# Kernel optimization log

Measured on AMD Instinct MI355X. Metric: run time of the kernel, lower is better.

## Reference

```python
import jax, jax.numpy as jnp
import numpy as np

B, T, C = 1, 2048, 2048
H, KH, HD = 16, 4, 128  # n_head, n_kv_head, head_dim
ROPE_BASE = 10000.0


def setup_inputs() -> dict:
    key = jax.random.key(0)
    ks = jax.random.split(key, 5)
    s = 0.02
    return {
        "x": jax.random.normal(ks[0], (B, T, C), jnp.float32),
        "Wq": jax.random.normal(ks[1], (C, H * HD), jnp.float32) * s,
        "Wk": jax.random.normal(ks[2], (C, KH * HD), jnp.float32) * s,
        "Wv": jax.random.normal(ks[3], (C, KH * HD), jnp.float32) * s,
        "Wo": jax.random.normal(ks[4], (H * HD, C), jnp.float32) * s,
        "position_ids": jnp.arange(T, dtype=jnp.int32),
    }


def _rotate_half(a):
    h = a.shape[-1] // 2
    return jnp.concatenate([-a[..., h:], a[..., :h]], axis=-1)


def reference(x, Wq, Wk, Wv, Wo, position_ids):
    b, t, c = x.shape
    n_rep = H // KH
    # projections -> [B, heads, T, HD]
    q = (x @ Wq).reshape(b, t, H, HD).transpose(0, 2, 1, 3)
    k = (x @ Wk).reshape(b, t, KH, HD).transpose(0, 2, 1, 3)
    v = (x @ Wv).reshape(b, t, KH, HD).transpose(0, 2, 1, 3)
    # rotary embedding cache [T, HD]
    inv_freq = 1.0 / (ROPE_BASE ** (jnp.arange(0, HD, 2, dtype=jnp.float32) / HD))
    pos = jnp.arange(t, dtype=jnp.float32)
    freqs = pos[:, None] * inv_freq[None, :]
    emb = jnp.concatenate([freqs, freqs], axis=-1)
    cos = jnp.cos(emb)[position_ids][None, None]  # [1,1,T,HD]
    sin = jnp.sin(emb)[position_ids][None, None]
    q = q * cos + _rotate_half(q) * sin
    k = k * cos + _rotate_half(k) * sin
    # GQA: group query heads instead of materializing repeated K/V
    qg = q.reshape(b, KH, n_rep, t, HD)
    scale = jnp.float32(1.0 / np.sqrt(HD))
    scores = jnp.einsum('bgrtd,bgsd->bgrts', qg, k) * scale
    causal = jnp.tril(jnp.ones((t, t), dtype=bool))
    scores = jnp.where(causal, scores, jnp.float32(-1e30))
    p = jax.nn.softmax(scores, axis=-1)
    y = jnp.einsum('bgrts,bgsd->bgrtd', p, v)
    y = y.reshape(b, H, t, HD).transpose(0, 2, 1, 3).reshape(b, t, H * HD)
    return y @ Wo
```

## Files before the change

kernel.cpp:

```cpp
#include <hip/hip_runtime.h>

typedef unsigned short u16;
using bf16x8 = __attribute__((ext_vector_type(8))) short;
using f32x4  = __attribute__((ext_vector_type(4))) float;

#define GLD16(g, l)                                                            \
  __builtin_amdgcn_global_load_lds(                                            \
      (const __attribute__((address_space(1))) void*)(g),                      \
      (__attribute__((address_space(3))) void*)(l), 16, 0, 0)

__device__ __forceinline__ u16 f2b(float x) {
  union { float f; unsigned u; } v; v.f = x;
  unsigned r = v.u + 0x7FFF + ((v.u >> 16) & 1);
  return (u16)(r >> 16);
}
__device__ __forceinline__ float b2f(u16 x) {
  union { unsigned u; float f; } v; v.u = (unsigned)x << 16; return v.f;
}

__global__ void cast_bf16_kernel(const float* __restrict__ in,
                                 u16* __restrict__ out, int n4) {
  int i = blockIdx.x * blockDim.x + threadIdx.x;
  int stride = gridDim.x * blockDim.x;
  for (; i < n4; i += stride) {
    float4 v = ((const float4*)in)[i];
    ushort4 o;
    o.x = f2b(v.x); o.y = f2b(v.y); o.z = f2b(v.z); o.w = f2b(v.w);
    ((ushort4*)out)[i] = o;
  }
}

__global__ void transpose_all_w_kernel(const float* __restrict__ Wq,
                                       const float* __restrict__ Wk,
                                       const float* __restrict__ Wv,
                                       const float* __restrict__ Wo,
                                       u16* __restrict__ Wqkv_bt,
                                       u16* __restrict__ Wo_bt) {
  __shared__ float tile[32][33];
  const int bx = blockIdx.x, k0 = blockIdx.y * 32;
  const int tx = threadIdx.x, ty = threadIdx.y;
  const float* src; int srcN, n0s; u16* dst; int dstRow0;
  if (bx < 64)      { src = Wq; srcN = 2048; n0s = bx * 32;        dst = Wqkv_bt; dstRow0 = bx * 32; }
  else if (bx < 80) { src = Wk; srcN = 512;  n0s = (bx - 64) * 32; dst = Wqkv_bt; dstRow0 = 2048 + (bx - 64) * 32; }
  else if (bx < 96) { src = Wv; srcN = 512;  n0s = (bx - 80) * 32; dst = Wqkv_bt; dstRow0 = 2560 + (bx - 80) * 32; }
  else              { src = Wo; srcN = 2048; n0s = (bx - 96) * 32; dst = Wo_bt;   dstRow0 = (bx - 96) * 32; }
#pragma unroll
  for (int r = 0; r < 4; r++)
    tile[ty + r * 8][tx] = src[(size_t)(k0 + ty + r * 8) * srcN + n0s + tx];
  __syncthreads();
#pragma unroll
  for (int r = 0; r < 4; r++)
    dst[(size_t)(dstRow0 + ty + r * 8) * 2048 + k0 + tx] = f2b(tile[tx][ty + r * 8]);
}

__global__ void transpose_v_kernel(const u16* __restrict__ src,
                                   u16* __restrict__ dst) {
  __shared__ u16 tile[32][33];
  int h = blockIdx.z;
  int t0 = blockIdx.x * 32, d0 = blockIdx.y * 32;
  const u16* s = src + (size_t)h * 2048 * 128;
  u16* d = dst + (size_t)h * 128 * 2048;
  int tx = threadIdx.x, ty = threadIdx.y;
#pragma unroll
  for (int r = 0; r < 4; r++)
    tile[ty + r * 8][tx] = s[(size_t)(t0 + ty + r * 8) * 128 + d0 + tx];
  __syncthreads();
#pragma unroll
  for (int r = 0; r < 4; r++)
    d[(size_t)(d0 + ty + r * 8) * 2048 + t0 + tx] = tile[tx][ty + r * 8];
}

__global__ __launch_bounds__(256, 2)
void gemm_bt_128(const u16* __restrict__ A, const u16* __restrict__ Bt,
                 float* __restrict__ C, int M, int N, int K) {
  __shared__ u16 As[4][128 * 32];
  __shared__ u16 Bs[4][128 * 32];
  const int tid = threadIdx.x;
  const int lane = tid & 63;
  const int w = tid >> 6;
  const int wr = w >> 1, wc = w & 1;
  const int m0 = blockIdx.y * 128, n0 = blockIdx.x * 128;

  f32x4 acc[4][4] = {};

  const int srow = tid >> 2, skg = tid & 3;
  const u16* Ag0 = A + (size_t)(m0 + srow) * K + skg * 8;
  const u16* Ag1 = A + (size_t)(m0 + 64 + srow) * K + skg * 8;
  const u16* Bg0 = Bt + (size_t)(n0 + srow) * K + skg * 8;
  const u16* Bg1 = Bt + (size_t)(n0 + 64 + srow) * K + skg * 8;

  const int l0 = tid * 8, l1 = (256 + tid) * 8;
  u16 *pa0 = As[0], *pa1 = As[1], *pa2 = As[2], *pa3 = As[3];
  u16 *pb0 = Bs[0], *pb1 = Bs[1], *pb2 = Bs[2], *pb3 = Bs[3];

#define GSTAGE(k0v, pa, pb)                                                    \
  {                                                                            \
    GLD16(Ag0 + (k0v), (pa) + l0);                                             \
    GLD16(Ag1 + (k0v), (pa) + l1);                                             \
    GLD16(Bg0 + (k0v), (pb) + l0);                                             \
    GLD16(Bg1 + (k0v), (pb) + l1);                                             \
  }

  GSTAGE(0, pa0, pb0);
  GSTAGE(32, pa1, pb1);

  const int frow = lane & 15, fk = (lane >> 4) * 8;
  const int nk = K >> 5;

  for (int i = 0; i < nk; ++i) {
    if (i + 2 < nk) {
      GSTAGE((i + 2) * 32, pa2, pb2);
      asm volatile("s_waitcnt vmcnt(8)" ::: "memory");
    } else if (i + 1 < nk) {
      asm volatile("s_waitcnt vmcnt(4)" ::: "memory");
    } else {
      asm volatile("s_waitcnt vmcnt(0)" ::: "memory");
    }
    __builtin_amdgcn_s_barrier();
    __builtin_amdgcn_sched_barrier(0);
    bf16x8 av[4], bv[4];
#pragma unroll
    for (int m = 0; m < 4; m++)
      av[m] = *(const bf16x8*)(pa0 + (wr * 64 + m * 16 + frow) * 32 + fk);
#pragma unroll
    for (int n = 0; n < 4; n++)
      bv[n] = *(const bf16x8*)(pb0 + (wc * 64 + n * 16 + frow) * 32 + fk);
#pragma unroll
    for (int m = 0; m < 4; m++)
#pragma unroll
      for (int n = 0; n < 4; n++)
        acc[m][n] =
            __builtin_amdgcn_mfma_f32_16x16x32_bf16(av[m], bv[n], acc[m][n], 0, 0, 0);
    u16* t;
    t = pa0; pa0 = pa1; pa1 = pa2; pa2 = pa3; pa3 = t;
    t = pb0; pb0 = pb1; pb1 = pb2; pb2 = pb3; pb3 = t;
  }
#undef GSTAGE

  const int crow = (lane >> 4) * 4, ccol = lane & 15;
#pragma unroll
  for (int m = 0; m < 4; m++)
#pragma unroll
    for (int n = 0; n < 4; n++)
#pragma unroll
      for (int r = 0; r < 4; r++)
        C[(size_t)(m0 + wr * 64 + m * 16 + crow + r) * N +
          (n0 + wc * 64 + n * 16 + ccol)] = acc[m][n][r];
}

__global__ void rope_kernel(const float* __restrict__ QKV,
                            const int* __restrict__ pos, u16* __restrict__ Qb,
                            u16* __restrict__ Kb, u16* __restrict__ Vb) {
  __shared__ float sc_[64], cc_[64];
  const int t = blockIdx.x, tid = threadIdx.x;
  const float p = (float)pos[t];
  const float* row = QKV + (size_t)t * 3072;
  const float qscale = 0.08838834764831845f;
  const float c0 = -0.015625f * 13.287712379549449f;
  if (tid < 64) {
    float ang = p * exp2f((float)tid * c0);
    sc_[tid] = sinf(ang);
    cc_[tid] = cosf(ang);
  }
  __syncthreads();
#pragma unroll
  for (int i = 0; i < 4; i++) {
    int idx = tid + i * 256;
    int head = idx >> 6, d = idx & 63;
    float s = sc_[d], c = cc_[d];
    float a0 = row[head * 128 + d], a1 = row[head * 128 + d + 64];
    Qb[((size_t)head * 2048 + t) * 128 + d] = f2b((a0 * c - a1 * s) * qscale);
    Qb[((size_t)head * 2048 + t) * 128 + d + 64] = f2b((a1 * c + a0 * s) * qscale);
  }
  {
    int head = tid >> 6, d = tid & 63;
    float s = sc_[d], c = cc_[d];
    float a0 = row[2048 + head * 128 + d], a1 = row[2048 + head * 128 + d + 64];
    Kb[((size_t)head * 2048 + t) * 128 + d] = f2b(a0 * c - a1 * s);
    Kb[((size_t)head * 2048 + t) * 128 + d + 64] = f2b(a1 * c + a0 * s);
  }
#pragma unroll
  for (int i = 0; i < 2; i++) {
    int e = tid + i * 256;
    int kh = e >> 7, d = e & 127;
    Vb[((size_t)kh * 2048 + t) * 128 + d] = f2b(row[2560 + e]);
  }
}

__global__ __launch_bounds__(256, 2)
void attn_kernel(const u16* __restrict__ Qb, const u16* __restrict__ Kb,
                 const u16* __restrict__ Vtb, u16* __restrict__ Op,
                 float* __restrict__ ml) {
  __shared__ u16 Ks[2][64 * 128];
  __shared__ u16 Vs[2][128 * 64];
  __shared__ u16 Ps[4][16 * 64];
  const int tid = threadIdx.x, lane = tid & 63, w = tid >> 6;
  const int h = blockIdx.y, g = h >> 2;
  const int z = blockIdx.z;
  const int frow = lane & 15, fgrp = lane >> 4;
  const int t0 = blockIdx.x;
  const int t1 = 31 - t0;
  const int c0 = (t0 >= z) ? ((t0 - z) >> 1) + 1 : 0;
  const int c1 = ((t1 - z) >> 1) + 1;
  const int nit = c0 + c1;

  const u16* Kg = Kb + (size_t)g * 2048 * 128;
  const u16* Vg = Vtb + (size_t)g * 128 * 2048;

#define STAGE(j0v, B)                                                          \
  {                                                                            \
    _Pragma("unroll")                                                          \
    for (int i = 0; i < 4; i++) {                                              \
      int p = tid + i * 256;                                                   \
      int kr = p >> 4, kc = (p & 15) ^ (kr & 7);                               \
      GLD16(Kg + (size_t)((j0v) + kr) * 128 + kc * 8, &Ks[B][p * 8]);          \
      int vr = p >> 3, vc = (p & 7) ^ (vr & 7);                                \
      GLD16(Vg + (size_t)vr * 2048 + (j0v) + vc * 8, &Vs[B][p * 8]);           \
    }                                                                          \
  }

#define FLUSH()                                                                \
  {                                                                            \
    _Pragma("unroll")                                                          \
    for (int r = 0; r < 4; r++) {                                              \
      float inv = lrow[r] > 0.f ? 1.0f / lrow[r] : 0.f;                        \
      int t = qw + fgrp * 4 + r;                                               \
      _Pragma("unroll")                                                        \
      for (int db = 0; db < 8; db++)                                           \
        Op[(size_t)z * 4194304 + (size_t)t * 2048 + h * 128 + db * 16 + frow] =\
            f2b(o[db][r] * inv);                                               \
      if (frow == 0) {                                                         \
        int mi = (((z * 16 + h) * 2048) + t) * 2;                              \
        ml[mi] = mrow[r]; ml[mi + 1] = lrow[r];                                \
      }                                                                        \
    }                                                                          \
  }

  int qw = t0 * 64 + w * 16;
  bf16x8 qf[4];
  {
    const u16* Qrow = Qb + ((size_t)h * 2048 + (qw + frow)) * 128 + fgrp * 8;
#pragma unroll
    for (int kf = 0; kf < 4; kf++) qf[kf] = *(const bf16x8*)(Qrow + kf * 32);
  }

  f32x4 o[8] = {};
  float mrow[4], lrow[4];
#pragma unroll
  for (int r = 0; r < 4; r++) { mrow[r] = -1e30f; lrow[r] = 0.f; }

  STAGE(z * 64, 0);
  __syncthreads();

  for (int it = 0; it < nit; ++it) {
    const int buf = it & 1;
    if (it + 1 < nit) {
      const int itn = it + 1;
      const int jn = (itn < c0) ? z + 2 * itn : z + 2 * (itn - c0);
      STAGE(jn * 64, buf ^ 1);
    }
    if (it == c0) {
      FLUSH();
#pragma unroll
      for (int db = 0; db < 8; db++)
#pragma unroll
        for (int r = 0; r < 4; r++) o[db][r] = 0.f;
#pragma unroll
      for (int r = 0; r < 4; r++) { mrow[r] = -1e30f; lrow[r] = 0.f; }
      qw = t1 * 64 + w * 16;
      const u16* Qrow = Qb + ((size_t)h * 2048 + (qw + frow)) * 128 + fgrp * 8;
#pragma unroll
      for (int kf = 0; kf < 4; kf++) qf[kf] = *(const bf16x8*)(Qrow + kf * 32);
    }
    const int pass = (it < c0) ? 0 : 1;
    const int j = (pass == 0) ? z + 2 * it : z + 2 * (it - c0);
    const bool diag = (pass == 0) ? (j == t0) : (j == t1);

    f32x4 sc[4] = {};
#pragma unroll
    for (int c = 0; c < 4; c++)
#pragma unroll
      for (int kf = 0; kf < 4; kf++) {
        int row = c * 16 + frow;
        bf16x8 kv = *(const bf16x8*)(
            &Ks[buf][row * 128 + ((kf * 4 + fgrp) ^ (row & 7)) * 8]);
        sc[c] = __builtin_amdgcn_mfma_f32_16x16x32_bf16(qf[kf], kv, sc[c], 0, 0, 0);
      }
    if (diag) {
#pragma unroll
      for (int c = 0; c < 4; c++) {
        int jj = c * 16 + frow;
#pragma unroll
        for (int r = 0; r < 4; r++)
          if (jj > (w * 16 + fgrp * 4 + r)) sc[c][r] = -1e30f;
      }
    }
    float pm[4];
#pragma unroll
    for (int r = 0; r < 4; r++)
      pm[r] = fmaxf(fmaxf(sc[0][r], sc[1][r]), fmaxf(sc[2][r], sc[3][r]));
#pragma unroll
    for (int off = 1; off < 16; off <<= 1)
#pragma unroll
      for (int r = 0; r < 4; r++) pm[r] = fmaxf(pm[r], __shfl_xor(pm[r], off, 64));
    bool nd = false;
#pragma unroll
    for (int r = 0; r < 4; r++) nd = nd || (pm[r] > mrow[r] + 8.f);
    if (__any(nd)) {
#pragma unroll
      for (int r = 0; r < 4; r++) {
        float mn = fmaxf(mrow[r], pm[r]);
        float alpha = __expf(mrow[r] - mn);
        mrow[r] = mn;
        lrow[r] *= alpha;
#pragma unroll
        for (int db = 0; db < 8; db++) o[db][r] *= alpha;
      }
    }
    float rs[4];
#pragma unroll
    for (int r = 0; r < 4; r++) {
      float s = 0.f;
#pragma unroll
      for (int c = 0; c < 4; c++) { sc[c][r] = __expf(sc[c][r] - mrow[r]); s += sc[c][r]; }
      rs[r] = s;
    }
#pragma unroll
    for (int off = 1; off < 16; off <<= 1)
#pragma unroll
      for (int r = 0; r < 4; r++) rs[r] += __shfl_xor(rs[r], off, 64);
#pragma unroll
    for (int r = 0; r < 4; r++) lrow[r] += rs[r];
    u16* Pw = Ps[w];
#pragma unroll
    for (int c = 0; c < 4; c++)
#pragma unroll
      for (int r = 0; r < 4; r++) {
        int row = fgrp * 4 + r, col = c * 16 + frow;
        Pw[row * 64 + (((col >> 3) ^ row) & 7) * 8 + (col & 7)] = f2b(sc[c][r]);
      }
    asm volatile("s_waitcnt lgkmcnt(0)" ::: "memory");
    bf16x8 pf[2];
#pragma unroll
    for (int ks = 0; ks < 2; ks++)
      pf[ks] = *(const bf16x8*)(
          &Pw[frow * 64 + ((ks * 4 + fgrp) ^ (frow & 7)) * 8]);
#pragma unroll
    for (int db = 0; db < 8; db++)
#pragma unroll
      for (int ks = 0; ks < 2; ks++) {
        int row = db * 16 + frow;
        bf16x8 vf = *(const bf16x8*)(
            &Vs[buf][row * 64 + ((ks * 4 + fgrp) ^ (row & 7)) * 8]);
        o[db] = __builtin_amdgcn_mfma_f32_16x16x32_bf16(pf[ks], vf, o[db], 0, 0, 0);
      }
    __syncthreads();
  }
  FLUSH();
#undef STAGE
#undef FLUSH
}

__global__ void attn_combine_kernel(const u16* __restrict__ Op,
                                    const float* __restrict__ ml,
                                    u16* __restrict__ Y) {
  int u = blockIdx.x * blockDim.x + threadIdx.x;
  int t = u >> 4, h = u & 15;
  int i0 = ((0 * 16 + h) * 2048 + t) * 2;
  int i1 = ((1 * 16 + h) * 2048 + t) * 2;
  float m0 = ml[i0], l0 = ml[i0 + 1];
  float m1 = ml[i1], l1 = ml[i1 + 1];
  float m = fmaxf(m0, m1);
  float w0 = __expf(m0 - m) * l0, w1 = __expf(m1 - m) * l1;
  float inv = 1.0f / (w0 + w1);
  w0 *= inv; w1 *= inv;
  size_t base = (size_t)t * 2048 + h * 128;
#pragma unroll
  for (int i = 0; i < 16; i++) {
    bf16x8 a = *(const bf16x8*)(Op + base + i * 8);
    bf16x8 b = *(const bf16x8*)(Op + 4194304 + base + i * 8);
    bf16x8 out;
#pragma unroll
    for (int jj = 0; jj < 8; jj++)
      out[jj] = (short)f2b(w0 * b2f((u16)a[jj]) + w1 * b2f((u16)b[jj]));
    *(bf16x8*)(Y + base + i * 8) = out;
  }
}

extern "C" void kernel_launch(void* const* d_in, const int* in_sizes, int n_in,
                              void* d_out, int out_size, void* d_ws,
                              size_t ws_size, hipStream_t stream) {
  const float* x  = (const float*)d_in[0];
  const float* Wq = (const float*)d_in[1];
  const float* Wk = (const float*)d_in[2];
  const float* Wv = (const float*)d_in[3];
  const float* Wo = (const float*)d_in[4];
  const int* pos  = (const int*)d_in[5];
  float* out = (float*)d_out;
  char* ws = (char*)d_ws;

  u16* xb      = (u16*)(ws + 0);
  u16* Wqkv_bt = (u16*)(ws + 8388608);
  u16* Wo_bt   = (u16*)(ws + 20971520);
  float* QKV   = (float*)(ws + 29360128);
  u16* Yb      = (u16*)(ws + 29360128);
  u16* Qb      = (u16*)(ws + 54525952);
  u16* Kb      = (u16*)(ws + 62914560);
  u16* Vb      = (u16*)(ws + 65011712);
  u16* Vtb     = (u16*)(ws + 67108864);
  u16* Op      = (u16*)(ws + 0);
  float* ml    = (float*)(ws + 16777216);

  cast_bf16_kernel<<<1024, 256, 0, stream>>>(x, xb, 2048 * 2048 / 4);
  transpose_all_w_kernel<<<dim3(160, 64), dim3(32, 8), 0, stream>>>(
      Wq, Wk, Wv, Wo, Wqkv_bt, Wo_bt);

  gemm_bt_128<<<dim3(3072 / 128, 2048 / 128), 256, 0, stream>>>(xb, Wqkv_bt, QKV, 2048, 3072, 2048);

  rope_kernel<<<2048, 256, 0, stream>>>(QKV, pos, Qb, Kb, Vb);
  transpose_v_kernel<<<dim3(64, 4, 4), dim3(32, 8), 0, stream>>>(Vb, Vtb);

  attn_kernel<<<dim3(16, 16, 2), 256, 0, stream>>>(Qb, Kb, Vtb, Op, ml);
  attn_combine_kernel<<<128, 256, 0, stream>>>(Op, ml, Yb);

  gemm_bt_128<<<dim3(2048 / 128, 2048 / 128), 256, 0, stream>>>(Yb, Wo_bt, out, 2048, 2048, 2048);
}
```

Baseline: 255.5 us.

## Fuse RoPE, scaling and bf16 cast into the QKV GEMM epilogue

Replaces the fp32 QKV GEMM plus separate rope kernel with a GEMM whose epilogue stages the tile in LDS, applies rotary embedding (using the partner column at col^64), applies the query scale, and writes bf16 Q/K/V directly in head-major layout. A precomputed cos/sin table, built inside the cast kernel, is read in the epilogue. This removes a 24MB fp32 intermediate write and read, and one kernel launch. In exchange the epilogue adds LDS traffic, scattered 2-byte stores and table reads.

```diff
diff --git a/kernel.cpp b/kernel.cpp
--- a/kernel.cpp
+++ b/kernel.cpp
@@ -19,10 +19,18 @@
 }
 
 __global__ void cast_bf16_kernel(const float* __restrict__ in,
-                                 u16* __restrict__ out, int n4) {
-  int i = blockIdx.x * blockDim.x + threadIdx.x;
+                                 u16* __restrict__ out, int n4,
+                                 const int* __restrict__ pos,
+                                 float2* __restrict__ tbl) {
+  int gid = blockIdx.x * blockDim.x + threadIdx.x;
   int stride = gridDim.x * blockDim.x;
-  for (; i < n4; i += stride) {
+  const float c0 = -0.015625f * 13.287712379549449f;
+  for (int j = gid; j < 2048 * 64; j += stride) {
+    int t = j >> 6, d = j & 63;
+    float ang = (float)pos[t] * exp2f((float)d * c0);
+    tbl[j] = make_float2(cosf(ang), sinf(ang));
+  }
+  for (int i = gid; i < n4; i += stride) {
     float4 v = ((const float4*)in)[i];
     ushort4 o;
     o.x = f2b(v.x); o.y = f2b(v.y); o.z = f2b(v.z); o.w = f2b(v.w);
@@ -71,6 +79,120 @@
 }
 
 __global__ __launch_bounds__(256, 2)
+void gemm_qkv_rope(const u16* __restrict__ A, const u16* __restrict__ Bt,
+                   const float2* __restrict__ tbl, u16* __restrict__ Qb,
+                   u16* __restrict__ Kb, u16* __restrict__ Vb) {
+  __shared__ u16 lds_[8][128 * 32];
+  const int K = 2048;
+  const int tid = threadIdx.x;
+  const int lane = tid & 63;
+  const int w = tid >> 6;
+  const int wr = w >> 1, wc = w & 1;
+  const int m0 = blockIdx.y * 128, n0 = blockIdx.x * 128;
+
+  f32x4 acc[4][4] = {};
+
+  const int srow = tid >> 2, skg = tid & 3;
+  const u16* Ag0 = A + (size_t)(m0 + srow) * K + skg * 8;
+  const u16* Ag1 = A + (size_t)(m0 + 64 + srow) * K + skg * 8;
+  const u16* Bg0 = Bt + (size_t)(n0 + srow) * K + skg * 8;
+  const u16* Bg1 = Bt + (size_t)(n0 + 64 + srow) * K + skg * 8;
+
+  const int l0 = tid * 8, l1 = (256 + tid) * 8;
+  u16 *pa0 = lds_[0], *pa1 = lds_[1], *pa2 = lds_[2], *pa3 = lds_[3];
+  u16 *pb0 = lds_[4], *pb1 = lds_[5], *pb2 = lds_[6], *pb3 = lds_[7];
+
+#define GSTAGE(k0v, pa, pb)                                                    \
+  {                                                                            \
+    GLD16(Ag0 + (k0v), (pa) + l0);                                             \
+    GLD16(Ag1 + (k0v), (pa) + l1);                                             \
+    GLD16(Bg0 + (k0v), (pb) + l0);                                             \
+    GLD16(Bg1 + (k0v), (pb) + l1);                                             \
+  }
+
+  GSTAGE(0, pa0, pb0);
+  GSTAGE(32, pa1, pb1);
+
+  const int frow = lane & 15, fk = (lane >> 4) * 8;
+  const int nk = K >> 5;
+
+  for (int i = 0; i < nk; ++i) {
+    if (i + 2 < nk) {
+      GSTAGE((i + 2) * 32, pa2, pb2);
+      asm volatile("s_waitcnt vmcnt(8)" ::: "memory");
+    } else if (i + 1 < nk) {
+      asm volatile("s_waitcnt vmcnt(4)" ::: "memory");
+    } else {
+      asm volatile("s_waitcnt vmcnt(0)" ::: "memory");
+    }
+    __builtin_amdgcn_s_barrier();
+    __builtin_amdgcn_sched_barrier(0);
+    bf16x8 av[4], bv[4];
+#pragma unroll
+    for (int m = 0; m < 4; m++)
+      av[m] = *(const bf16x8*)(pa0 + (wr * 64 + m * 16 + frow) * 32 + fk);
+#pragma unroll
+    for (int n = 0; n < 4; n++)
+      bv[n] = *(const bf16x8*)(pb0 + (wc * 64 + n * 16 + frow) * 32 + fk);
+#pragma unroll
+    for (int m = 0; m < 4; m++)
+#pragma unroll
+      for (int n = 0; n < 4; n++)
+        acc[m][n] =
+            __builtin_amdgcn_mfma_f32_16x16x32_bf16(av[m], bv[n], acc[m][n], 0, 0, 0);
+    u16* t;
+    t = pa0; pa0 = pa1; pa1 = pa2; pa2 = pa3; pa3 = t;
+    t = pb0; pb0 = pb1; pb1 = pb2; pb2 = pb3; pb3 = t;
+  }
+#undef GSTAGE
+
+  const int crow = (lane >> 4) * 4, ccol = lane & 15;
+  if (n0 < 2560) {
+    __syncthreads();
+    float* S = (float*)lds_;
+#pragma unroll
+    for (int m = 0; m < 4; m++)
+#pragma unroll
+      for (int n = 0; n < 4; n++)
+#pragma unroll
+        for (int r = 0; r < 4; r++)
+          S[(wr * 64 + m * 16 + crow + r) * 128 + wc * 64 + n * 16 + ccol] =
+              acc[m][n][r];
+    __syncthreads();
+    const bool isQ = (n0 < 2048);
+    u16* dst = isQ ? Qb + (size_t)(n0 >> 7) * 2048 * 128
+                   : Kb + (size_t)((n0 - 2048) >> 7) * 2048 * 128;
+    const float sgn = (wc == 0) ? -1.f : 1.f;
+    const float qs = isQ ? 0.08838834764831845f : 1.0f;
+#pragma unroll
+    for (int m = 0; m < 4; m++)
+#pragma unroll
+      for (int n = 0; n < 4; n++)
+#pragma unroll
+        for (int r = 0; r < 4; r++) {
+          int row = wr * 64 + m * 16 + crow + r;
+          int col = wc * 64 + n * 16 + ccol;
+          int t = m0 + row, d = col & 63;
+          float2 cs = tbl[t * 64 + d];
+          float val = acc[m][n][r] * cs.x + sgn * S[row * 128 + (col ^ 64)] * cs.y;
+          dst[(size_t)t * 128 + col] = f2b(val * qs);
+        }
+  } else {
+    u16* dst = Vb + (size_t)((n0 - 2560) >> 7) * 2048 * 128;
+#pragma unroll
+    for (int m = 0; m < 4; m++)
+#pragma unroll
+      for (int n = 0; n < 4; n++)
+#pragma unroll
+        for (int r = 0; r < 4; r++) {
+          int row = wr * 64 + m * 16 + crow + r;
+          int col = wc * 64 + n * 16 + ccol;
+          dst[(size_t)(m0 + row) * 128 + col] = f2b(acc[m][n][r]);
+        }
+  }
+}
+
+__global__ __launch_bounds__(256, 2)
 void gemm_bt_128(const u16* __restrict__ A, const u16* __restrict__ Bt,
                  float* __restrict__ C, int M, int N, int K) {
   __shared__ u16 As[4][128 * 32];
@@ -146,45 +268,6 @@
       for (int r = 0; r < 4; r++)
         C[(size_t)(m0 + wr * 64 + m * 16 + crow + r) * N +
           (n0 + wc * 64 + n * 16 + ccol)] = acc[m][n][r];
-}
-
-__global__ void rope_kernel(const float* __restrict__ QKV,
-                            const int* __restrict__ pos, u16* __restrict__ Qb,
-                            u16* __restrict__ Kb, u16* __restrict__ Vb) {
-  __shared__ float sc_[64], cc_[64];
-  const int t = blockIdx.x, tid = threadIdx.x;
-  const float p = (float)pos[t];
-  const float* row = QKV + (size_t)t * 3072;
-  const float qscale = 0.08838834764831845f;
-  const float c0 = -0.015625f * 13.287712379549449f;
-  if (tid < 64) {
-    float ang = p * exp2f((float)tid * c0);
-    sc_[tid] = sinf(ang);
-    cc_[tid] = cosf(ang);
-  }
-  __syncthreads();
-#pragma unroll
-  for (int i = 0; i < 4; i++) {
-    int idx = tid + i * 256;
-    int head = idx >> 6, d = idx & 63;
-    float s = sc_[d], c = cc_[d];
-    float a0 = row[head * 128 + d], a1 = row[head * 128 + d + 64];
-    Qb[((size_t)head * 2048 + t) * 128 + d] = f2b((a0 * c - a1 * s) * qscale);
-    Qb[((size_t)head * 2048 + t) * 128 + d + 64] = f2b((a1 * c + a0 * s) * qscale);
-  }
-  {
-    int head = tid >> 6, d = tid & 63;
-    float s = sc_[d], c = cc_[d];
-    float a0 = row[2048 + head * 128 + d], a1 = row[2048 + head * 128 + d + 64];
-    Kb[((size_t)head * 2048 + t) * 128 + d] = f2b(a0 * c - a1 * s);
-    Kb[((size_t)head * 2048 + t) * 128 + d + 64] = f2b(a1 * c + a0 * s);
-  }
-#pragma unroll
-  for (int i = 0; i < 2; i++) {
-    int e = tid + i * 256;
-    int kh = e >> 7, d = e & 127;
-    Vb[((size_t)kh * 2048 + t) * 128 + d] = f2b(row[2560 + e]);
-  }
 }
 
 __global__ __launch_bounds__(256, 2)
@@ -402,8 +485,8 @@
   u16* xb      = (u16*)(ws + 0);
   u16* Wqkv_bt = (u16*)(ws + 8388608);
   u16* Wo_bt   = (u16*)(ws + 20971520);
-  float* QKV   = (float*)(ws + 29360128);
-  u16* Yb      = (u16*)(ws + 29360128);
+  float2* tbl  = (float2*)(ws + 29360128);
+  u16* Yb      = (u16*)(ws + 31457280);
   u16* Qb      = (u16*)(ws + 54525952);
   u16* Kb      = (u16*)(ws + 62914560);
   u16* Vb      = (u16*)(ws + 65011712);
@@ -411,13 +494,12 @@
   u16* Op      = (u16*)(ws + 0);
   float* ml    = (float*)(ws + 16777216);
 
-  cast_bf16_kernel<<<1024, 256, 0, stream>>>(x, xb, 2048 * 2048 / 4);
+  cast_bf16_kernel<<<1024, 256, 0, stream>>>(x, xb, 2048 * 2048 / 4, pos, tbl);
   transpose_all_w_kernel<<<dim3(160, 64), dim3(32, 8), 0, stream>>>(
       Wq, Wk, Wv, Wo, Wqkv_bt, Wo_bt);
 
-  gemm_bt_128<<<dim3(3072 / 128, 2048 / 128), 256, 0, stream>>>(xb, Wqkv_bt, QKV, 2048, 3072, 2048);
-
-  rope_kernel<<<2048, 256, 0, stream>>>(QKV, pos, Qb, Kb, Vb);
+  gemm_qkv_rope<<<dim3(24, 16), 256, 0, stream>>>(xb, Wqkv_bt, tbl, Qb, Kb, Vb);
+
   transpose_v_kernel<<<dim3(64, 4, 4), dim3(32, 8), 0, stream>>>(Vb, Vtb);
 
   attn_kernel<<<dim3(16, 16, 2), 256, 0, stream>>>(Qb, Kb, Vtb, Op, ml);
```

Result: faster. 242.2 us (-5.2%).
